# Performance work log

Measured on AMD Instinct MI355X. Metric: run time of the kernel, lower is better.

## Reference

```python
import jax, jax.numpy as jnp
import numpy as np

T_STEPS = 32      # discrete samples along each pixel's voting ray
RAY_STEP = 4.0    # pixel stride between ray samples


def setup_inputs() -> dict:
    key = jax.random.key(0)
    k1, k2, k3, k4 = jax.random.split(key, 4)
    B, C, H, W = 2, 22, 480, 640
    label = jax.random.randint(k1, (B, H, W), 0, C, dtype=jnp.int32)
    vertex = jax.random.normal(k2, (B, 3 * C, H, W), dtype=jnp.float32)
    # per-class 3D extents in meters (~0..0.3 m objects)
    extents = jax.random.uniform(k3, (C, 3), dtype=jnp.float32) * 0.3
    # flattened intrinsics [fx, 0, cx, 0, fy, cy, 0, 0, 1]
    intr = jnp.array([572.4, 0.0, 325.3, 0.0, 573.6, 242.0, 0.0, 0.0, 1.0], dtype=jnp.float32)
    meta_data = jnp.tile(intr[None, :], (B, 1))
    gt = jax.random.normal(k4, (B, C, 4, 4), dtype=jnp.float32)
    return {"label": label, "vertex": vertex, "extents": extents,
            "meta_data": meta_data, "gt": gt, "is_train": 0}


def reference(label, vertex, extents, meta_data, gt, is_train):
    B, C3, H, W = vertex.shape
    C = C3 // 3
    HW = H * W
    f32 = jnp.float32

    # Gather each pixel's class-specific vertex prediction: (nx, ny, z)
    v = vertex.reshape(B, C, 3, HW)                        # (B,C,3,HW)
    lab = label.reshape(B, HW)                             # (B,HW) int
    idx = jnp.broadcast_to(lab[:, None, None, :], (B, 1, 3, HW))
    g = jnp.take_along_axis(v, idx, axis=1)[:, 0]          # (B,3,HW)
    nx, ny, z = g[:, 0], g[:, 1], g[:, 2]
    inv_norm = 1.0 / (jnp.sqrt(nx * nx + ny * ny) + 1e-8)
    nx = nx * inv_norm
    ny = ny * inv_norm

    # Pixel coordinates
    pix = jnp.arange(HW, dtype=jnp.int32)
    xs = (pix % W).astype(f32)
    ys = (pix // W).astype(f32)

    # Cast T_STEPS votes along the predicted ray toward the object center
    t = (jnp.arange(1, T_STEPS + 1, dtype=f32) * RAY_STEP)  # (T,)
    px = jnp.round(xs[None, :, None] + nx[:, :, None] * t[None, None, :]).astype(jnp.int32)
    py = jnp.round(ys[None, :, None] + ny[:, :, None] * t[None, None, :]).astype(jnp.int32)
    inb = (px >= 0) & (px < W) & (py >= 0) & (py < H)
    fg = (lab > 0)[:, :, None]                              # background casts no votes
    w = (inb & fg).astype(f32)                              # (B,HW,T)
    flat = jnp.clip(py, 0, H - 1) * W + jnp.clip(px, 0, W - 1)

    # Scatter-accumulate votes into per-class Hough space (B,C,HW)
    b_idx = jnp.arange(B)[:, None, None]
    acc = jnp.zeros((B, C, HW), dtype=f32).at[b_idx, lab[:, :, None], flat].add(w)

    # Peak detection: argmax per (batch, class)
    peak = jnp.argmax(acc, axis=-1)                         # (B,C)
    votes = jnp.max(acc, axis=-1)                           # (B,C)
    cx = (peak % W).astype(f32)
    cy = (peak // W).astype(f32)

    # Mean predicted depth per class (masked mean over that class's pixels)
    b2 = jnp.arange(B)[:, None]
    cnt = jnp.zeros((B, C), dtype=f32).at[b2, lab].add(1.0)
    zsum = jnp.zeros((B, C), dtype=f32).at[b2, lab].add(z)
    depth = zsum / jnp.maximum(cnt, 1.0)

    # Project object extents to image-plane box size: half = 0.5*|extent|*fx/depth
    fx = meta_data[:, 0][:, None]                           # (B,1)
    diag = jnp.linalg.norm(extents, axis=-1)[None, :]       # (1,C)
    half = 0.5 * diag * fx / jnp.maximum(jnp.abs(depth), 1e-3)

    cls = jnp.broadcast_to(jnp.arange(C, dtype=f32)[None, :], (B, C))
    out = jnp.stack([cls, votes,
                     cx - half, cy - half, cx + half, cy + half,
                     cx, cy, depth], axis=-1)               # (B,C,9)
    return out
```

## Files before the change

### kernel.cpp

```cpp
#include <hip/hip_runtime.h>


#define MAXC 32

__global__ __launch_bounds__(512) void emit_kernel(
    const int* __restrict__ label, const float* __restrict__ vertex,
    unsigned short* __restrict__ bucketData, unsigned* __restrict__ cursor,
    unsigned* __restrict__ cnt, float* __restrict__ zsum,
    int C, int H, int W, int HW, int CAP)
{
    __shared__ unsigned s_bin[512];
    __shared__ unsigned s_pos[512];
    __shared__ unsigned s_gbase[512];
    __shared__ unsigned short s_buf[16384];
    __shared__ unsigned s_wtot[8];
    __shared__ unsigned s_ccnt[MAXC];
    __shared__ float s_cz[MAXC];

    int tid = threadIdx.x;
    int lane = tid & 63, wave = tid >> 6;
    int b = blockIdx.y;
    int p = blockIdx.x * 512 + tid;

    s_bin[tid] = 0;
    if (tid < MAXC) { s_ccnt[tid] = 0u; s_cz[tid] = 0.0f; }
    __syncthreads();

    int lab = 0;
    unsigned vote[32];
    bool fg = false;
    if (p < HW) {
        lab = label[(size_t)b * HW + p];
        const float* vbase = vertex + (size_t)b * 3 * C * HW + p;
        float nx = 0.f, ny = 0.f, z = 0.f;
        #pragma unroll 2
        for (int c = 0; c < C; ++c) {
            float v0 = vbase[(size_t)(3 * c + 0) * HW];
            float v1 = vbase[(size_t)(3 * c + 1) * HW];
            float v2 = vbase[(size_t)(3 * c + 2) * HW];
            if (lab == c) { nx = v0; ny = v1; z = v2; }
        }
        atomicAdd(&s_ccnt[lab], 1u);
        atomicAdd(&s_cz[lab], z);
        if (lab > 0) {
            fg = true;
            float nrm = __fsqrt_rn(__fadd_rn(__fmul_rn(nx, nx), __fmul_rn(ny, ny)));
            float inv = __fdiv_rn(1.0f, __fadd_rn(nrm, 1e-8f));
            float nxn = __fmul_rn(nx, inv);
            float nyn = __fmul_rn(ny, inv);
            float xs = (float)(p % W);
            float ys = (float)(p / W);
            #pragma unroll
            for (int i = 1; i <= 32; ++i) {
                float t = (float)i * 4.0f;
                int px = (int)rintf(__fadd_rn(xs, __fmul_rn(nxn, t)));
                int py = (int)rintf(__fadd_rn(ys, __fmul_rn(nyn, t)));
                vote[i - 1] = (px >= 0 && px < W && py >= 0 && py < H)
                            ? ((unsigned)(py << 10) | (unsigned)px) : 0xFFFFFFFFu;
            }
        }
    }
    if (!fg) {
        #pragma unroll
        for (int i = 0; i < 32; ++i) vote[i] = 0xFFFFFFFFu;
    }

    #pragma unroll
    for (int i = 0; i < 32; ++i)
        if (vote[i] != 0xFFFFFFFFu) atomicAdd(&s_bin[vote[i] >> 10], 1u);
    __syncthreads();

    unsigned own = s_bin[tid];
    unsigned v = own;
    #pragma unroll
    for (int off = 1; off < 64; off <<= 1) {
        unsigned u = __shfl_up(v, off, 64);
        if (lane >= off) v += u;
    }
    if (lane == 63) s_wtot[wave] = v;

    unsigned resN = (tid < H) ? s_bin[tid] : 0u;
    unsigned resBase = resN ? atomicAdd(&cursor[b * H + tid], resN) : 0u;

    __syncthreads();
    if (tid == 0) {
        unsigned a = 0;
        #pragma unroll
        for (int w2 = 0; w2 < 8; ++w2) { unsigned t2 = s_wtot[w2]; s_wtot[w2] = a; a += t2; }
    }
    if (tid < H) s_gbase[tid] = resBase;
    __syncthreads();
    s_pos[tid] = v + s_wtot[wave] - own;
    __syncthreads();

    #pragma unroll
    for (int i = 0; i < 32; ++i) {
        unsigned vt = vote[i];
        if (vt != 0xFFFFFFFFu) {
            unsigned slot = atomicAdd(&s_pos[vt >> 10], 1u);
            s_buf[slot] = (unsigned short)(((unsigned)lab << 10) | (vt & 1023u));
        }
    }
    __syncthreads();

    for (int y = wave; y < H; y += 8) {
        unsigned n = s_bin[y];
        if (!n) continue;
        unsigned ebase = s_pos[y] - n;
        unsigned gbase = s_gbase[y];
        unsigned short* dst = bucketData + (size_t)(b * H + y) * CAP;
        for (unsigned i = (unsigned)lane; i < n; i += 64) {
            unsigned g = gbase + i;
            if (g < (unsigned)CAP) dst[g] = s_buf[ebase + i];
        }
    }

    if (tid < C) {
        unsigned c = s_ccnt[tid];
        if (c) {
            atomicAdd(&cnt[b * C + tid], c);
            atomicAdd(&zsum[b * C + tid], s_cz[tid]);
        }
    }
}

__global__ __launch_bounds__(256) void hist_kernel(
    const unsigned short* __restrict__ bucketData,
    const unsigned* __restrict__ cursor,
    unsigned long long* __restrict__ keys,
    int C, int H, int W, int CAP)
{
    extern __shared__ char sm[];
    unsigned* hist = (unsigned*)sm;
    unsigned long long* s_wb =
        (unsigned long long*)(sm + (size_t)(C * W / 2) * 4);

    int tid = threadIdx.x;
    int lane = tid & 63, wave = tid >> 6;
    int py = blockIdx.x;
    int b = blockIdx.y;
    int words = C * W / 2;

    for (int i = tid; i < words; i += 256) hist[i] = 0u;
    __syncthreads();

    int bucket = b * H + py;
    unsigned n = cursor[bucket];
    if (n > (unsigned)CAP) n = (unsigned)CAP;
    const unsigned short* src = bucketData + (size_t)bucket * CAP;
    for (unsigned i = tid; i < n; i += 256) {
        unsigned r = src[i];
        unsigned idx = (r >> 10) * (unsigned)W + (r & 1023u);
        atomicAdd(&hist[idx >> 1], 1u << ((idx & 1u) * 16));
    }
    __syncthreads();

    unsigned rowbase = (unsigned)py * (unsigned)W;
    for (int c = 0; c < C; ++c) {
        unsigned long long best = 0;
        for (int px = tid; px < W; px += 256) {
            unsigned cv = (hist[(unsigned)(c * W + px) >> 1] >> ((px & 1) * 16)) & 0xFFFFu;
            unsigned long long k = ((unsigned long long)cv << 32)
                                 | (unsigned long long)(0xFFFFFFFFu - (rowbase + px));
            if (k > best) best = k;
        }
        #pragma unroll
        for (int off = 32; off > 0; off >>= 1) {
            unsigned long long o = __shfl_xor(best, off, 64);
            if (o > best) best = o;
        }
        if (lane == 0) s_wb[c * 4 + wave] = best;
    }
    __syncthreads();
    if (tid < C) {
        unsigned long long m = s_wb[tid * 4];
        #pragma unroll
        for (int w2 = 1; w2 < 4; ++w2)
            if (s_wb[tid * 4 + w2] > m) m = s_wb[tid * 4 + w2];
        atomicMax(&keys[b * C + tid], m);
    }
}

__global__ void finalize_kernel(const unsigned long long* __restrict__ keys,
                                const unsigned* __restrict__ cnt,
                                const float* __restrict__ zsum,
                                const float* __restrict__ extents,
                                const float* __restrict__ meta,
                                float* __restrict__ out,
                                int B, int C, int W)
{
    int i = threadIdx.x;
    if (i >= B * C) return;
    int b = i / C, c = i % C;
    unsigned long long k = keys[i];
    unsigned votes = (unsigned)(k >> 32);
    unsigned peak = 0xFFFFFFFFu - (unsigned)(k & 0xFFFFFFFFull);
    float cx = (float)(peak % (unsigned)W);
    float cy = (float)(peak / (unsigned)W);
    float n = (float)cnt[i];
    float depth = zsum[i] / fmaxf(n, 1.0f);
    float fx = meta[b * 9 + 0];
    const float* e = extents + c * 3;
    float diag = sqrtf(e[0] * e[0] + e[1] * e[1] + e[2] * e[2]);
    float half = 0.5f * diag * fx / fmaxf(fabsf(depth), 0.001f);
    float* o = out + (size_t)i * 9;
    o[0] = (float)c;
    o[1] = (float)votes;
    o[2] = cx - half;
    o[3] = cy - half;
    o[4] = cx + half;
    o[5] = cy + half;
    o[6] = cx;
    o[7] = cy;
    o[8] = depth;
}

extern "C" void kernel_launch(void* const* d_in, const int* in_sizes, int n_in,
                              void* d_out, int out_size, void* d_ws, size_t ws_size,
                              hipStream_t stream)
{
    const int* label    = (const int*)d_in[0];
    const float* vertex = (const float*)d_in[1];
    const float* extents= (const float*)d_in[2];
    const float* meta   = (const float*)d_in[3];

    int C = in_sizes[2] / 3;
    int B = in_sizes[3] / 9;
    int HW = in_sizes[0] / B;
    const int W = 640;
    int H = HW / W;
    int NB = B * H;

    size_t keysOff = 0;
    size_t curOff  = keysOff + (size_t)B * C * 8;
    size_t cntOff  = curOff + (size_t)NB * 4;
    size_t zsumOff = cntOff + (size_t)B * C * 4;
    size_t zeroEnd = zsumOff + (size_t)B * C * 4;
    size_t dataOff = (zeroEnd + 63) & ~(size_t)63;

    size_t availRec = (ws_size > dataOff) ? (ws_size - dataOff) / ((size_t)NB * 2) : 0;
    int CAP = (int)(availRec > 32768 ? 32768 : availRec);
    CAP &= ~63;

    unsigned long long* keys = (unsigned long long*)((char*)d_ws + keysOff);
    unsigned* cursor         = (unsigned*)((char*)d_ws + curOff);
    unsigned* cnt            = (unsigned*)((char*)d_ws + cntOff);
    float* zsum              = (float*)((char*)d_ws + zsumOff);
    unsigned short* bucketData = (unsigned short*)((char*)d_ws + dataOff);

    hipMemsetAsync(d_ws, 0, zeroEnd, stream);

    dim3 egrid((HW + 511) / 512, B);
    emit_kernel<<<egrid, 512, 0, stream>>>(label, vertex, bucketData, cursor,
                                           cnt, zsum, C, H, W, HW, CAP);

    dim3 hgrid(H, B);
    size_t hsm = (size_t)(C * W / 2) * 4 + (size_t)C * 4 * 8;
    hist_kernel<<<hgrid, 256, hsm, stream>>>(bucketData, cursor, keys, C, H, W, CAP);

    finalize_kernel<<<1, 64, 0, stream>>>(keys, cnt, zsum, extents, meta,
                                          (float*)d_out, B, C, W);
}
```

Baseline: 120.3 us.

## Halve emit block size and recompute ray votes instead of holding them in registers

The emit kernel now runs 256-thread blocks with half the shared staging buffer, and each thread scans two row bins in the prefix sum. It no longer keeps a 32-entry vote array in registers; the ray samples are computed once to build the row histogram and again to scatter entries. This is meant to cut register pressure and shared memory per block so more blocks fit per CU, at the cost of repeating the ray arithmetic and issuing more global cursor atomics because there are twice as many blocks.

```diff
diff --git a/kernel.cpp b/kernel.cpp
--- a/kernel.cpp
+++ b/kernel.cpp
@@ -3,7 +3,7 @@
 
 #define MAXC 32
 
-__global__ __launch_bounds__(512) void emit_kernel(
+__global__ __launch_bounds__(256) void emit_kernel(
     const int* __restrict__ label, const float* __restrict__ vertex,
     unsigned short* __restrict__ bucketData, unsigned* __restrict__ cursor,
     unsigned* __restrict__ cnt, float* __restrict__ zsum,
@@ -12,23 +12,24 @@
     __shared__ unsigned s_bin[512];
     __shared__ unsigned s_pos[512];
     __shared__ unsigned s_gbase[512];
-    __shared__ unsigned short s_buf[16384];
-    __shared__ unsigned s_wtot[8];
+    __shared__ unsigned short s_buf[8192];
+    __shared__ unsigned s_wtot[4];
     __shared__ unsigned s_ccnt[MAXC];
     __shared__ float s_cz[MAXC];
 
     int tid = threadIdx.x;
     int lane = tid & 63, wave = tid >> 6;
     int b = blockIdx.y;
-    int p = blockIdx.x * 512 + tid;
+    int p = blockIdx.x * 256 + tid;
 
     s_bin[tid] = 0;
+    s_bin[tid + 256] = 0;
     if (tid < MAXC) { s_ccnt[tid] = 0u; s_cz[tid] = 0.0f; }
     __syncthreads();
 
     int lab = 0;
-    unsigned vote[32];
     bool fg = false;
+    float nxn = 0.f, nyn = 0.f, xs = 0.f, ys = 0.f;
     if (p < HW) {
         lab = label[(size_t)b * HW + p];
         const float* vbase = vertex + (size_t)b * 3 * C * HW + p;
@@ -46,72 +47,76 @@
             fg = true;
             float nrm = __fsqrt_rn(__fadd_rn(__fmul_rn(nx, nx), __fmul_rn(ny, ny)));
             float inv = __fdiv_rn(1.0f, __fadd_rn(nrm, 1e-8f));
-            float nxn = __fmul_rn(nx, inv);
-            float nyn = __fmul_rn(ny, inv);
-            float xs = (float)(p % W);
-            float ys = (float)(p / W);
-            #pragma unroll
-            for (int i = 1; i <= 32; ++i) {
-                float t = (float)i * 4.0f;
-                int px = (int)rintf(__fadd_rn(xs, __fmul_rn(nxn, t)));
-                int py = (int)rintf(__fadd_rn(ys, __fmul_rn(nyn, t)));
-                vote[i - 1] = (px >= 0 && px < W && py >= 0 && py < H)
-                            ? ((unsigned)(py << 10) | (unsigned)px) : 0xFFFFFFFFu;
-            }
-        }
-    }
-    if (!fg) {
-        #pragma unroll
-        for (int i = 0; i < 32; ++i) vote[i] = 0xFFFFFFFFu;
-    }
-
-    #pragma unroll
-    for (int i = 0; i < 32; ++i)
-        if (vote[i] != 0xFFFFFFFFu) atomicAdd(&s_bin[vote[i] >> 10], 1u);
-    __syncthreads();
-
-    unsigned own = s_bin[tid];
-    unsigned v = own;
+            nxn = __fmul_rn(nx, inv);
+            nyn = __fmul_rn(ny, inv);
+            xs = (float)(p % W);
+            ys = (float)(p / W);
+        }
+    }
+
+    if (fg) {
+        #pragma unroll
+        for (int i = 1; i <= 32; ++i) {
+            float t = (float)i * 4.0f;
+            int px = (int)rintf(__fadd_rn(xs, __fmul_rn(nxn, t)));
+            int py = (int)rintf(__fadd_rn(ys, __fmul_rn(nyn, t)));
+            if (px >= 0 && px < W && py >= 0 && py < H)
+                atomicAdd(&s_bin[py], 1u);
+        }
+    }
+    __syncthreads();
+
+    unsigned b0 = s_bin[2 * tid], b1 = s_bin[2 * tid + 1];
+    unsigned pairsum = b0 + b1;
+    unsigned v = pairsum;
     #pragma unroll
     for (int off = 1; off < 64; off <<= 1) {
         unsigned u = __shfl_up(v, off, 64);
         if (lane >= off) v += u;
     }
     if (lane == 63) s_wtot[wave] = v;
-
-    unsigned resN = (tid < H) ? s_bin[tid] : 0u;
-    unsigned resBase = resN ? atomicAdd(&cursor[b * H + tid], resN) : 0u;
-
     __syncthreads();
     if (tid == 0) {
         unsigned a = 0;
         #pragma unroll
-        for (int w2 = 0; w2 < 8; ++w2) { unsigned t2 = s_wtot[w2]; s_wtot[w2] = a; a += t2; }
-    }
-    if (tid < H) s_gbase[tid] = resBase;
-    __syncthreads();
-    s_pos[tid] = v + s_wtot[wave] - own;
-    __syncthreads();
-
-    #pragma unroll
-    for (int i = 0; i < 32; ++i) {
-        unsigned vt = vote[i];
-        if (vt != 0xFFFFFFFFu) {
-            unsigned slot = atomicAdd(&s_pos[vt >> 10], 1u);
-            s_buf[slot] = (unsigned short)(((unsigned)lab << 10) | (vt & 1023u));
-        }
-    }
-    __syncthreads();
-
-    for (int y = wave; y < H; y += 8) {
+        for (int w2 = 0; w2 < 4; ++w2) { unsigned t2 = s_wtot[w2]; s_wtot[w2] = a; a += t2; }
+    }
+    __syncthreads();
+    unsigned ebase0 = v + s_wtot[wave] - pairsum;
+    s_pos[2 * tid]     = ebase0;
+    s_pos[2 * tid + 1] = ebase0 + b0;
+
+    int y0 = 2 * tid, y1 = 2 * tid + 1;
+    unsigned g0 = 0, g1 = 0;
+    if (y0 < H && b0) g0 = atomicAdd(&cursor[b * H + y0], b0);
+    if (y1 < H && b1) g1 = atomicAdd(&cursor[b * H + y1], b1);
+    s_gbase[y0] = g0;
+    s_gbase[y1] = g1;
+    __syncthreads();
+
+    if (fg) {
+        #pragma unroll
+        for (int i = 1; i <= 32; ++i) {
+            float t = (float)i * 4.0f;
+            int px = (int)rintf(__fadd_rn(xs, __fmul_rn(nxn, t)));
+            int py = (int)rintf(__fadd_rn(ys, __fmul_rn(nyn, t)));
+            if (px >= 0 && px < W && py >= 0 && py < H) {
+                unsigned slot = atomicAdd(&s_pos[py], 1u);
+                s_buf[slot] = (unsigned short)(((unsigned)lab << 10) | (unsigned)px);
+            }
+        }
+    }
+    __syncthreads();
+
+    for (int y = wave; y < H; y += 4) {
         unsigned n = s_bin[y];
         if (!n) continue;
-        unsigned ebase = s_pos[y] - n;
-        unsigned gbase = s_gbase[y];
+        unsigned eb = s_pos[y] - n;
+        unsigned gb = s_gbase[y];
         unsigned short* dst = bucketData + (size_t)(b * H + y) * CAP;
         for (unsigned i = (unsigned)lane; i < n; i += 64) {
-            unsigned g = gbase + i;
-            if (g < (unsigned)CAP) dst[g] = s_buf[ebase + i];
+            unsigned g = gb + i;
+            if (g < (unsigned)CAP) dst[g] = s_buf[eb + i];
         }
     }
 
@@ -250,8 +255,8 @@
 
     hipMemsetAsync(d_ws, 0, zeroEnd, stream);
 
-    dim3 egrid((HW + 511) / 512, B);
-    emit_kernel<<<egrid, 512, 0, stream>>>(label, vertex, bucketData, cursor,
+    dim3 egrid((HW + 255) / 256, B);
+    emit_kernel<<<egrid, 256, 0, stream>>>(label, vertex, bucketData, cursor,
                                            cnt, zsum, C, H, W, HW, CAP);
 
     dim3 hgrid(H, B);
```

New measurement: 178.7 us. +48.6%, slower.
